# Performance work log

Measured on AMD Instinct MI355X. Metric: run time of the kernel, lower is better.

## Reference

```python
import jax, jax.numpy as jnp
import numpy as np

DIM = 384
NUM_HEADS = 12
KERNEL = 3
DILATIONS = (1, 2, 3)
B, H, W = 16, 56, 56


def _unfold(x, k, dil):
    # x: [B, c, H, W] -> [B, c, k*k, H, W]; matches nn.Unfold(k, dilation=dil,
    # padding=dil*(k-1)//2, stride=1) channel ordering [c, kh, kw].
    b, c, h, w = x.shape
    p = dil * (k - 1) // 2
    xp = jnp.pad(x, ((0, 0), (0, 0), (p, p), (p, p)))
    patches = [xp[:, :, i * dil:i * dil + h, j * dil:j * dil + w]
               for i in range(k) for j in range(k)]
    return jnp.stack(patches, axis=2)


def _dilate_attention(q, k, v, head_dim, kernel, dil):
    # q,k,v: [B, c, H, W]
    b, c, h, w = q.shape
    g = c // head_dim           # heads in this dilation branch
    kk = kernel * kernel
    scale = head_dim ** (-0.5)
    qg = q.reshape(b, g, head_dim, h * w)                       # [b,g,d,n]
    ku = _unfold(k, kernel, dil).reshape(b, g, head_dim, kk, h * w)
    vu = _unfold(v, kernel, dil).reshape(b, g, head_dim, kk, h * w)
    attn = jnp.einsum('bgdn,bgdkn->bgnk', qg, ku) * scale       # [b,g,n,kk]
    attn = jax.nn.softmax(attn, axis=-1)
    out = jnp.einsum('bgnk,bgdkn->bgnd', attn, vu)              # [b,g,n,d]
    return out.transpose(0, 2, 1, 3).reshape(b, h, w, c)        # [b,h,w,c]


def setup_inputs() -> dict:
    key = jax.random.key(0)
    kx, kq, kp = jax.random.split(key, 3)
    x = jax.random.normal(kx, (B, H, W, DIM), dtype=jnp.float32)
    w_qkv = jax.random.normal(kq, (3 * DIM, DIM), dtype=jnp.float32) * 0.02
    w_proj = jax.random.normal(kp, (DIM, DIM), dtype=jnp.float32) * 0.02
    b_proj = jnp.zeros((DIM,), dtype=jnp.float32)
    return {"x": x, "w_qkv": w_qkv, "w_proj": w_proj, "b_proj": b_proj}


def reference(x, w_qkv, w_proj, b_proj):
    b, h, w, c = x.shape
    nd = len(DILATIONS)
    cg = c // nd                # channels per dilation branch
    hd = c // NUM_HEADS         # head_dim
    xc = x.transpose(0, 3, 1, 2)                                 # [b,c,h,w]
    qkv = jnp.einsum('bchw,oc->bohw', xc, w_qkv)                 # 1x1 conv, no bias
    qkv = qkv.reshape(b, 3, nd, cg, h, w)
    outs = [_dilate_attention(qkv[:, 0, i], qkv[:, 1, i], qkv[:, 2, i],
                              hd, KERNEL, DILATIONS[i]) for i in range(nd)]
    y = jnp.stack(outs, axis=3).reshape(b, h, w, c)              # [b,h,w, nd*cg]
    return jnp.einsum('bhwc,oc->bhwo', y, w_proj) + b_proj
```

## Files before the change

kernel.cpp:

```cpp
#include <hip/hip_runtime.h>
#include <hip/hip_bf16.h>


#define NTOK 50176
#define ROWQKV 1152
#define CDIM 384

typedef _Float16 half2v __attribute__((ext_vector_type(2)));
typedef _Float16 half8 __attribute__((ext_vector_type(8)));
typedef float floatx4 __attribute__((ext_vector_type(4)));

typedef __attribute__((address_space(1))) const unsigned int GU32;
typedef __attribute__((address_space(3))) unsigned int LU32;

#define N_X4 (NTOK * CDIM / 4)
#define N_Q4 (ROWQKV * CDIM / 4)
#define N_P4 (CDIM * CDIM / 4)

__global__ __launch_bounds__(256) void conv_all(const float* __restrict__ x,
                                                const float* __restrict__ wq,
                                                const float* __restrict__ wp,
                                                _Float16* __restrict__ xh,
                                                _Float16* __restrict__ wqh,
                                                _Float16* __restrict__ wph) {
  const int total = N_X4 + N_Q4 + N_P4;
  int i = blockIdx.x * 256 + threadIdx.x;
  const int stride = gridDim.x * 256;
  for (; i < total; i += stride) {
    const float* src;
    _Float16* dst;
    int k;
    if (i < N_X4) { src = x; dst = xh; k = i; }
    else if (i < N_X4 + N_Q4) { src = wq; dst = wqh; k = i - N_X4; }
    else { src = wp; dst = wph; k = i - N_X4 - N_Q4; }
    float4 v = ((const float4*)src)[k];
    union { _Float16 h[4]; uint2 u; } o;
    o.h[0] = (_Float16)v.x; o.h[1] = (_Float16)v.y;
    o.h[2] = (_Float16)v.z; o.h[3] = (_Float16)v.w;
    ((uint2*)dst)[k] = o.u;
  }
}

template <bool HALF_OUT>
__global__ __launch_bounds__(256) void gemm3(const _Float16* __restrict__ A,
                                             const _Float16* __restrict__ B,
                                             const float* __restrict__ bias,
                                             void* __restrict__ Cout,
                                             int N, int K) {
  __shared__ _Float16 Asl[2][128 * 32];
  __shared__ _Float16 Bsl[2][128 * 32];
  const int tid = threadIdx.x;
  const int lane = tid & 63;
  const int wv = tid >> 6;
  const int wr = wv >> 1, wc = wv & 1;

  const int nN = N >> 7;
  const int p = blockIdx.x;
  const int l = (p & 7) * (gridDim.x >> 3) + (p >> 3);
  const size_t row0 = (size_t)(l / nN) * 128;
  const int col0 = (l % nN) * 128;
  const int NT = K / 32;

  const int srow = tid >> 2;
  const int gslot = (tid & 3) ^ ((srow >> 1) & 3);
  const _Float16* Abase = A + (row0 + srow) * (size_t)K + gslot * 8;
  const _Float16* Bbase = B + ((size_t)(col0 + srow)) * (size_t)K + gslot * 8;
  char* AsB = (char*)Asl;
  char* BsB = (char*)Bsl;

  auto stage = [&](int k0, int buf) {
    __builtin_amdgcn_global_load_lds((GU32*)(Abase + k0),
                                     (LU32*)(AsB + buf * 8192 + tid * 16), 16, 0, 0);
    __builtin_amdgcn_global_load_lds((GU32*)(Abase + (size_t)64 * K + k0),
                                     (LU32*)(AsB + buf * 8192 + tid * 16 + 4096), 16, 0, 0);
    __builtin_amdgcn_global_load_lds((GU32*)(Bbase + k0),
                                     (LU32*)(BsB + buf * 8192 + tid * 16), 16, 0, 0);
    __builtin_amdgcn_global_load_lds((GU32*)(Bbase + (size_t)64 * K + k0),
                                     (LU32*)(BsB + buf * 8192 + tid * 16 + 4096), 16, 0, 0);
  };

  const int fr = lane & 15;
  const int fq = lane >> 4;
  const int rpos = (fq ^ ((fr >> 1) & 3)) * 8;

  floatx4 acc[4][4];
#pragma unroll
  for (int i = 0; i < 4; ++i)
#pragma unroll
    for (int j = 0; j < 4; ++j) acc[i][j] = (floatx4){0.f, 0.f, 0.f, 0.f};

  stage(0, 0);
  asm volatile("s_waitcnt vmcnt(0)" ::: "memory");
  __builtin_amdgcn_s_barrier();

  int cur = 0;
  for (int t = 0; t < NT; ++t) {
    if (t + 1 < NT) {
      stage((t + 1) * 32, cur ^ 1);
      asm volatile("s_waitcnt vmcnt(4)" ::: "memory");
    } else {
      asm volatile("s_waitcnt vmcnt(0)" ::: "memory");
    }
    __builtin_amdgcn_s_barrier();
    __builtin_amdgcn_sched_barrier(0);
    half8 af[4], bf[4];
#pragma unroll
    for (int f = 0; f < 4; ++f) {
      af[f] = *(const half8*)&Asl[cur][(wr * 64 + f * 16 + fr) * 32 + rpos];
      bf[f] = *(const half8*)&Bsl[cur][(wc * 64 + f * 16 + fr) * 32 + rpos];
    }
#pragma unroll
    for (int i = 0; i < 4; ++i)
#pragma unroll
      for (int j = 0; j < 4; ++j)
        acc[i][j] = __builtin_amdgcn_mfma_f32_16x16x32_f16(af[i], bf[j], acc[i][j], 0, 0, 0);
    __builtin_amdgcn_sched_barrier(0);
    __builtin_amdgcn_s_barrier();
    cur ^= 1;
  }

  const int crow = wr * 64 + (lane >> 4) * 4;
  const int ccol = wc * 64 + (lane & 15);
#pragma unroll
  for (int fm = 0; fm < 4; ++fm) {
#pragma unroll
    for (int fn = 0; fn < 4; ++fn) {
      const size_t r0 = (row0 + crow + fm * 16) * (size_t)N + col0 + ccol + fn * 16;
      if (HALF_OUT) {
        _Float16* Cc = (_Float16*)Cout;
#pragma unroll
        for (int j = 0; j < 4; ++j) Cc[r0 + (size_t)j * N] = (_Float16)acc[fm][fn][j];
      } else {
        float* Cc = (float*)Cout;
        const float bz = bias[col0 + ccol + fn * 16];
#pragma unroll
        for (int j = 0; j < 4; ++j) Cc[r0 + (size_t)j * N] = acc[fm][fn][j] + bz;
      }
    }
  }
}

template <int DIL>
__global__ __launch_bounds__(256) void attn_tile(const _Float16* __restrict__ qkv,
                                                 _Float16* __restrict__ y) {
  constexpr int H = 8 + 2 * DIL;
  constexpr int NROW = H * H;
  __shared__ char kv[NROW * 560];
  const int tid = threadIdx.x;
  const int head = tid & 3;
  const int tok = tid >> 2;
  const int ly = tok >> 3, lx = tok & 7;
  const int branch = DIL - 1;
  const int cb = branch * 128;
  const int bimg = blockIdx.y;
  const int ty0 = (blockIdx.x / 7) * 8;
  const int tx0 = (blockIdx.x % 7) * 8;
  const size_t base = (size_t)bimg * 3136;
  const float scale = 0.17677669529663687f;

  constexpr int NG = NROW * 32;
  for (int g = tid; g < NG; g += 256) {
    const int r = g >> 5, sl = g & 31;
    const int gy = ty0 - DIL + r / H;
    const int gx = tx0 - DIL + r % H;
    uint4 val = make_uint4(0u, 0u, 0u, 0u);
    if ((unsigned)gy < 56u && (unsigned)gx < 56u) {
      const int off = (sl < 16) ? (384 + cb + sl * 8) : (768 + cb + (sl - 16) * 8);
      val = *(const uint4*)(qkv + (base + gy * 56 + gx) * ROWQKV + off);
    }
    *(uint4*)(kv + r * 560 + sl * 16) = val;
  }

  const int gty = ty0 + ly, gtx = tx0 + lx;
  const _Float16* qp = qkv + (base + gty * 56 + gtx) * ROWQKV + cb + head * 32;
  half2v qh[16];
  *(half8*)&qh[0] = *(const half8*)(qp);
  *(half8*)&qh[4] = *(const half8*)(qp + 8);
  *(half8*)&qh[8] = *(const half8*)(qp + 16);
  *(half8*)&qh[12] = *(const half8*)(qp + 24);

  __syncthreads();

  int rtap[9];
#pragma unroll
  for (int j = 0; j < 9; ++j) {
    const int dy = j / 3 - 1, dx = j % 3 - 1;
    rtap[j] = (ly + DIL + dy * DIL) * H + (lx + DIL + dx * DIL);
  }

  float l[9];
#pragma unroll
  for (int j = 0; j < 9; ++j) {
    const char* kp = kv + rtap[j] * 560 + head * 64;
    half2v kh[16];
    *(half8*)&kh[0] = *(const half8*)(kp);
    *(half8*)&kh[4] = *(const half8*)(kp + 16);
    *(half8*)&kh[8] = *(const half8*)(kp + 32);
    *(half8*)&kh[12] = *(const half8*)(kp + 48);
    float d = 0.f;
#if __has_builtin(__builtin_amdgcn_fdot2)
#pragma unroll
    for (int c = 0; c < 16; ++c) d = __builtin_amdgcn_fdot2(qh[c], kh[c], d, false);
#else
#pragma unroll
    for (int c = 0; c < 16; ++c)
      d += (float)qh[c][0] * (float)kh[c][0] + (float)qh[c][1] * (float)kh[c][1];
#endif
    l[j] = d * scale;
  }

  float m = l[0];
#pragma unroll
  for (int j = 1; j < 9; ++j) m = fmaxf(m, l[j]);
  float s = 0.f;
#pragma unroll
  for (int j = 0; j < 9; ++j) { l[j] = expf(l[j] - m); s += l[j]; }
  const float rs = 1.f / s;

  float out[32];
#pragma unroll
  for (int c = 0; c < 32; ++c) out[c] = 0.f;
#pragma unroll
  for (int j = 0; j < 9; ++j) {
    const char* vp = kv + rtap[j] * 560 + 256 + head * 64;
    half8 vh[4];
    vh[0] = *(const half8*)(vp);
    vh[1] = *(const half8*)(vp + 16);
    vh[2] = *(const half8*)(vp + 32);
    vh[3] = *(const half8*)(vp + 48);
    const float p = l[j];
#pragma unroll
    for (int g = 0; g < 4; ++g)
#pragma unroll
      for (int e = 0; e < 8; ++e) out[g * 8 + e] = fmaf(p, (float)vh[g][e], out[g * 8 + e]);
  }

  _Float16* yp = y + (base + gty * 56 + gtx) * (size_t)CDIM + cb + head * 32;
  half8 oh[4];
#pragma unroll
  for (int g = 0; g < 4; ++g) {
#pragma unroll
    for (int e = 0; e < 8; ++e) oh[g][e] = (_Float16)(out[g * 8 + e] * rs);
    *(half8*)(yp + g * 8) = oh[g];
  }
}

extern "C" void kernel_launch(void* const* d_in, const int* in_sizes, int n_in,
                              void* d_out, int out_size, void* d_ws, size_t ws_size,
                              hipStream_t stream) {
  const float* x = (const float*)d_in[0];
  const float* w_qkv = (const float*)d_in[1];
  const float* w_proj = (const float*)d_in[2];
  const float* b_proj = (const float*)d_in[3];
  float* out = (float*)d_out;

  _Float16* xh = (_Float16*)d_ws;
  _Float16* wqh = xh + (size_t)NTOK * CDIM;
  _Float16* wph = wqh + (size_t)ROWQKV * CDIM;
  _Float16* qkvh = wph + (size_t)CDIM * CDIM;
  _Float16* yh = qkvh + (size_t)NTOK * ROWQKV;

  conv_all<<<2048, 256, 0, stream>>>(x, w_qkv, w_proj, xh, wqh, wph);

  gemm3<true><<<(NTOK / 128) * (ROWQKV / 128), 256, 0, stream>>>(
      xh, wqh, nullptr, qkvh, ROWQKV, CDIM);

  attn_tile<1><<<dim3(49, 16), 256, 0, stream>>>(qkvh, yh);
  attn_tile<2><<<dim3(49, 16), 256, 0, stream>>>(qkvh, yh);
  attn_tile<3><<<dim3(49, 16), 256, 0, stream>>>(qkvh, yh);

  gemm3<false><<<(NTOK / 128) * (CDIM / 128), 256, 0, stream>>>(
      yh, wph, b_proj, out, CDIM, CDIM);
}
```

Measured before the change: 214.4 us.

## Merge dilation attention launches and stage K then V through halved LDS

Replaces the three per-dilation attention launches with one kernel whose block index is remapped (interleaved by 8) onto branch, image and tile, with dilation now a runtime value. K is loaded into shared memory first, and after the logits are computed the same buffer is refilled with V. This halves the LDS footprint so more blocks can be resident per CU and saves two launches. In exchange it adds two extra barriers, serialises the V load after the QK pass, and loses compile-time constants for the tile geometry.

```diff
diff --git a/kernel.cpp b/kernel.cpp
--- a/kernel.cpp
+++ b/kernel.cpp
@@ -140,36 +140,25 @@
   }
 }
 
-template <int DIL>
-__global__ __launch_bounds__(256) void attn_tile(const _Float16* __restrict__ qkv,
-                                                 _Float16* __restrict__ y) {
-  constexpr int H = 8 + 2 * DIL;
-  constexpr int NROW = H * H;
-  __shared__ char kv[NROW * 560];
+__global__ __launch_bounds__(256) void attn_tile2(const _Float16* __restrict__ qkv,
+                                                  _Float16* __restrict__ y) {
+  __shared__ char kv[196 * 272];
+  const int p = blockIdx.x;
+  const int l = (p & 7) * 294 + (p >> 3);
+  const int branch = l / 784;
+  const int rem = l - branch * 784;
+  const int bimg = rem / 49;
+  const int tile = rem - bimg * 49;
+  const int dil = branch + 1;
+  const int H = 8 + 2 * dil;
+  const int NROW = H * H;
+  const int cb = branch * 128;
+  const int ty0 = (tile / 7) * 8, tx0 = (tile % 7) * 8;
   const int tid = threadIdx.x;
-  const int head = tid & 3;
-  const int tok = tid >> 2;
+  const int head = tid & 3, tok = tid >> 2;
   const int ly = tok >> 3, lx = tok & 7;
-  const int branch = DIL - 1;
-  const int cb = branch * 128;
-  const int bimg = blockIdx.y;
-  const int ty0 = (blockIdx.x / 7) * 8;
-  const int tx0 = (blockIdx.x % 7) * 8;
   const size_t base = (size_t)bimg * 3136;
   const float scale = 0.17677669529663687f;
-
-  constexpr int NG = NROW * 32;
-  for (int g = tid; g < NG; g += 256) {
-    const int r = g >> 5, sl = g & 31;
-    const int gy = ty0 - DIL + r / H;
-    const int gx = tx0 - DIL + r % H;
-    uint4 val = make_uint4(0u, 0u, 0u, 0u);
-    if ((unsigned)gy < 56u && (unsigned)gx < 56u) {
-      const int off = (sl < 16) ? (384 + cb + sl * 8) : (768 + cb + (sl - 16) * 8);
-      val = *(const uint4*)(qkv + (base + gy * 56 + gx) * ROWQKV + off);
-    }
-    *(uint4*)(kv + r * 560 + sl * 16) = val;
-  }
 
   const int gty = ty0 + ly, gtx = tx0 + lx;
   const _Float16* qp = qkv + (base + gty * 56 + gtx) * ROWQKV + cb + head * 32;
@@ -179,19 +168,30 @@
   *(half8*)&qh[8] = *(const half8*)(qp + 16);
   *(half8*)&qh[12] = *(const half8*)(qp + 24);
 
+  const int NG = NROW * 16;
+
+  for (int g = tid; g < NG; g += 256) {
+    const int r = g >> 4, sl = g & 15;
+    const int gy = ty0 - dil + r / H;
+    const int gx = tx0 - dil + r % H;
+    uint4 val = make_uint4(0u, 0u, 0u, 0u);
+    if ((unsigned)gy < 56u && (unsigned)gx < 56u)
+      val = *(const uint4*)(qkv + (base + gy * 56 + gx) * ROWQKV + 384 + cb + sl * 8);
+    *(uint4*)(kv + r * 272 + sl * 16) = val;
+  }
   __syncthreads();
 
   int rtap[9];
 #pragma unroll
   for (int j = 0; j < 9; ++j) {
     const int dy = j / 3 - 1, dx = j % 3 - 1;
-    rtap[j] = (ly + DIL + dy * DIL) * H + (lx + DIL + dx * DIL);
-  }
-
-  float l[9];
+    rtap[j] = (ly + dil + dy * dil) * H + (lx + dil + dx * dil);
+  }
+
+  float lg[9];
 #pragma unroll
   for (int j = 0; j < 9; ++j) {
-    const char* kp = kv + rtap[j] * 560 + head * 64;
+    const char* kp = kv + rtap[j] * 272 + head * 64;
     half2v kh[16];
     *(half8*)&kh[0] = *(const half8*)(kp);
     *(half8*)&kh[4] = *(const half8*)(kp + 16);
@@ -206,33 +206,46 @@
     for (int c = 0; c < 16; ++c)
       d += (float)qh[c][0] * (float)kh[c][0] + (float)qh[c][1] * (float)kh[c][1];
 #endif
-    l[j] = d * scale;
-  }
-
-  float m = l[0];
-#pragma unroll
-  for (int j = 1; j < 9; ++j) m = fmaxf(m, l[j]);
+    lg[j] = d * scale;
+  }
+  __syncthreads();
+
+  for (int g = tid; g < NG; g += 256) {
+    const int r = g >> 4, sl = g & 15;
+    const int gy = ty0 - dil + r / H;
+    const int gx = tx0 - dil + r % H;
+    uint4 val = make_uint4(0u, 0u, 0u, 0u);
+    if ((unsigned)gy < 56u && (unsigned)gx < 56u)
+      val = *(const uint4*)(qkv + (base + gy * 56 + gx) * ROWQKV + 768 + cb + sl * 8);
+    *(uint4*)(kv + r * 272 + sl * 16) = val;
+  }
+
+  float m = lg[0];
+#pragma unroll
+  for (int j = 1; j < 9; ++j) m = fmaxf(m, lg[j]);
   float s = 0.f;
 #pragma unroll
-  for (int j = 0; j < 9; ++j) { l[j] = expf(l[j] - m); s += l[j]; }
+  for (int j = 0; j < 9; ++j) { lg[j] = expf(lg[j] - m); s += lg[j]; }
   const float rs = 1.f / s;
 
+  __syncthreads();
+
   float out[32];
 #pragma unroll
   for (int c = 0; c < 32; ++c) out[c] = 0.f;
 #pragma unroll
   for (int j = 0; j < 9; ++j) {
-    const char* vp = kv + rtap[j] * 560 + 256 + head * 64;
+    const char* vp = kv + rtap[j] * 272 + head * 64;
     half8 vh[4];
     vh[0] = *(const half8*)(vp);
     vh[1] = *(const half8*)(vp + 16);
     vh[2] = *(const half8*)(vp + 32);
     vh[3] = *(const half8*)(vp + 48);
-    const float p = l[j];
+    const float pw = lg[j];
 #pragma unroll
     for (int g = 0; g < 4; ++g)
 #pragma unroll
-      for (int e = 0; e < 8; ++e) out[g * 8 + e] = fmaf(p, (float)vh[g][e], out[g * 8 + e]);
+      for (int e = 0; e < 8; ++e) out[g * 8 + e] = fmaf(pw, (float)vh[g][e], out[g * 8 + e]);
   }
 
   _Float16* yp = y + (base + gty * 56 + gtx) * (size_t)CDIM + cb + head * 32;
@@ -265,9 +278,7 @@
   gemm3<true><<<(NTOK / 128) * (ROWQKV / 128), 256, 0, stream>>>(
       xh, wqh, nullptr, qkvh, ROWQKV, CDIM);
 
-  attn_tile<1><<<dim3(49, 16), 256, 0, stream>>>(qkvh, yh);
-  attn_tile<2><<<dim3(49, 16), 256, 0, stream>>>(qkvh, yh);
-  attn_tile<3><<<dim3(49, 16), 256, 0, stream>>>(qkvh, yh);
+  attn_tile2<<<2352, 256, 0, stream>>>(qkvh, yh);
 
   gemm3<false><<<(NTOK / 128) * (CDIM / 128), 256, 0, stream>>>(
       yh, wph, b_proj, out, CDIM, CDIM);
```

Measured after the change: 191.1 us. -10.9%, faster.
